# Kernel tuning notes

Hardware: AMD Instinct MI355X
Metric: run time of the kernel (lower is better)

## Reference

```python
import jax, jax.numpy as jnp
import numpy as np

D = 1024
N_HEAD = 16
D_HEAD = D // N_HEAD
EPS = 1e-6


def setup_inputs() -> dict:
    key = jax.random.key(0)
    k1, k2, k3 = jax.random.split(key, 3)
    x = jax.random.normal(k1, (4, 1024, D), dtype=jnp.float32)
    # Linear weights stored as (in, out); y = x @ W
    Wqkv = jax.random.normal(k2, (D, 3 * D), dtype=jnp.float32) * (1.0 / np.sqrt(D))
    Wo = jax.random.normal(k3, (D, D), dtype=jnp.float32) * (1.0 / np.sqrt(D))
    scale_q = jnp.ones((D_HEAD,), dtype=jnp.float32)
    scale_k = jnp.ones((D_HEAD,), dtype=jnp.float32)
    return {"x": x, "Wqkv": Wqkv, "Wo": Wo, "scale_q": scale_q, "scale_k": scale_k}


def _rmsnorm_global(x, scale):
    # NOTE: faithful to source: mean over ALL elements (scalar RMS), not per-vector.
    rms = jnp.sqrt(jnp.mean(x * x))
    return (x / (rms + EPS)) * scale  # scale broadcasts over last dim (d_head)


def reference(x, Wqkv, Wo, scale_q, scale_k):
    b, s, d = x.shape
    qkv = x @ Wqkv  # (b, s, 3d)
    q, k, v = jnp.split(qkv, 3, axis=-1)
    q = q.reshape(b, s, N_HEAD, D_HEAD)
    k = k.reshape(b, s, N_HEAD, D_HEAD)
    v = v.reshape(b, s, N_HEAD, D_HEAD)
    q = _rmsnorm_global(q, scale_q)
    k = _rmsnorm_global(k, scale_k)
    # NOTE: no 1/sqrt(d_head) scaling, no mask (faithful to source)
    attn = jnp.einsum('bqhd,bkhd->bhqk', q, k)
    attn = jax.nn.softmax(attn, axis=-1)
    z = jnp.einsum('bhqk,bkhd->bqhd', attn, v)
    z = z.reshape(b, s, d)
    return z @ Wo
```

## Files before the change

### kernel.cpp

```cpp
#include <hip/hip_runtime.h>

typedef float f32x4 __attribute__((ext_vector_type(4)));
typedef short bf16x8 __attribute__((ext_vector_type(8)));
typedef _Float16 f16x8 __attribute__((ext_vector_type(8)));
typedef unsigned short u16;

__device__ __forceinline__ u16 f2bf(float f) {
  unsigned int u = __float_as_uint(f);
  u = u + 0x7fffu + ((u >> 16) & 1u);
  return (u16)(u >> 16);
}
__device__ __forceinline__ float bf2f(u16 h) {
  return __uint_as_float(((unsigned int)h) << 16);
}
__device__ __forceinline__ u16 f2h(float f) {
  _Float16 h = (_Float16)f;
  union { _Float16 h; u16 u; } cv;
  cv.h = h;
  return cv.u;
}

typedef unsigned int as1_uint __attribute__((address_space(1)));
typedef unsigned int as3_uint __attribute__((address_space(3)));
__device__ __forceinline__ void gl_lds16(const void* g, void* l) {
  __builtin_amdgcn_global_load_lds((as1_uint*)g, (as3_uint*)l, 16, 0, 0);
}


__global__ __launch_bounds__(256) void conv_x_kernel(const float* __restrict__ x,
                                                     u16* __restrict__ Xp) {
  const int g = blockIdx.x * 256 + threadIdx.x;
  const int o = g * 8;
  const int slab = o >> 17;
  const int rem = o & 131071;
  const int kstep = rem >> 12;
  const int rem2 = rem & 4095;
  const int r = rem2 >> 5;
  const int cp = (rem2 & 31) >> 3;
  const int c = cp ^ ((r >> 1) & 3);
  const int s = slab * 128 + r;
  const int k = kstep * 32 + c * 8;
  const float4 v0 = *(const float4*)&x[(size_t)s * 1024 + k];
  const float4 v1 = *(const float4*)&x[(size_t)s * 1024 + k + 4];
  ushort4 a, b;
  a.x = f2h(v0.x); a.y = f2h(v0.y); a.z = f2h(v0.z); a.w = f2h(v0.w);
  b.x = f2h(v1.x); b.y = f2h(v1.y); b.z = f2h(v1.z); b.w = f2h(v1.w);
  *(ushort4*)&Xp[o] = a;
  *(ushort4*)&Xp[o + 4] = b;
}

__global__ __launch_bounds__(256) void conv_w_kernel(
    const float* __restrict__ src, int ncols, u16* __restrict__ dst) {
  __shared__ float tl[64][132];
  const int t = threadIdx.x;
  const int slab = blockIdx.x, kg = blockIdx.y;
  const int n0 = slab * 128, k0 = kg * 64;
#pragma unroll
  for (int i = 0; i < 8; i++) {
    const int fidx = i * 256 + t;
    const int r = fidx >> 5, c4 = (fidx & 31) * 4;
    *(float4*)&tl[r][c4] = *(const float4*)&src[(size_t)(k0 + r) * ncols + n0 + c4];
  }
  __syncthreads();
  const size_t base = (size_t)slab * 131072 + (size_t)(kg * 2) * 4096;
#pragma unroll
  for (int i = 0; i < 4; i++) {
    const int g = i * 256 + t;
    const int img = g >> 9, ci = g & 511;
    const int r = ci >> 2, cp = ci & 3;
    const int c = cp ^ ((r >> 1) & 3);
    const int klc = img * 32 + c * 8;
    ushort4 h0, h1;
    float v[8];
#pragma unroll
    for (int e = 0; e < 8; e++) v[e] = tl[klc + e][r];
    h0.x = f2h(v[0]); h0.y = f2h(v[1]); h0.z = f2h(v[2]); h0.w = f2h(v[3]);
    h1.x = f2h(v[4]); h1.y = f2h(v[5]); h1.z = f2h(v[6]); h1.w = f2h(v[7]);
    *(ushort4*)&dst[base + g * 8] = h0;
    *(ushort4*)&dst[base + g * 8 + 4] = h1;
  }
}

__global__ __launch_bounds__(256) void gemm_qkv_kernel(
    const u16* __restrict__ Xp, const u16* __restrict__ Wp,
    u16* __restrict__ qf, u16* __restrict__ kf, u16* __restrict__ vT,
    const float* __restrict__ scale_q, const float* __restrict__ scale_k,
    float* __restrict__ sums) {
  __shared__ u16 Xs0[4096], Ws0[4096], Xs1[4096], Ws1[4096];
  const int tid = threadIdx.x, wv = tid >> 6, lane = tid & 63;
  const int lm = lane & 15, quad = lane >> 4;
  const int bnS = blockIdx.x, bmS = blockIdx.y;
  const bool is_v = (bnS >= 16);
  const int wr = (wv >> 1) * 64, wc = (wv & 1) * 64;
  const int fq = (quad ^ ((lm >> 1) & 3)) * 8;
  const u16* Xg = Xp + (size_t)bmS * 131072;
  const u16* Wg = Wp + (size_t)bnS * 131072;
  const int dof0 = (wv * 2) * 512, dof1 = (wv * 2 + 1) * 512;
  const f32x4 z4 = {0.f, 0.f, 0.f, 0.f};
  f32x4 acc[4][4];
#pragma unroll
  for (int i = 0; i < 4; i++)
#pragma unroll
    for (int j = 0; j < 4; j++) acc[i][j] = z4;

#define ISSUE(t, Xs, Ws)                                   \
  do {                                                     \
    const size_t tb_ = (size_t)(t) * 4096;                 \
    gl_lds16(Xg + tb_ + dof0 + lane * 8, &Xs[dof0]);       \
    gl_lds16(Xg + tb_ + dof1 + lane * 8, &Xs[dof1]);       \
    gl_lds16(Wg + tb_ + dof0 + lane * 8, &Ws[dof0]);       \
    gl_lds16(Wg + tb_ + dof1 + lane * 8, &Ws[dof1]);       \
  } while (0)

  const u16* A0 = is_v ? Xs0 : Ws0;
  const u16* B0 = is_v ? Ws0 : Xs0;
  const u16* A1 = is_v ? Xs1 : Ws1;
  const u16* B1 = is_v ? Ws1 : Xs1;

  ISSUE(0, Xs0, Ws0);
  for (int t = 0; t < 32; t += 2) {
    __syncthreads();
    {
      f16x8 afr[4], bfr[4];
#pragma unroll
      for (int mi = 0; mi < 4; mi++)
        afr[mi] = *(const f16x8*)&A0[(wr + mi * 16 + lm) * 32 + fq];
#pragma unroll
      for (int ni = 0; ni < 4; ni++)
        bfr[ni] = *(const f16x8*)&B0[(wc + ni * 16 + lm) * 32 + fq];
      ISSUE(t + 1, Xs1, Ws1);
#pragma unroll
      for (int mi = 0; mi < 4; mi++)
#pragma unroll
        for (int ni = 0; ni < 4; ni++)
          acc[mi][ni] = __builtin_amdgcn_mfma_f32_16x16x32_f16(
              afr[mi], bfr[ni], acc[mi][ni], 0, 0, 0);
    }
    __syncthreads();
    {
      f16x8 afr[4], bfr[4];
#pragma unroll
      for (int mi = 0; mi < 4; mi++)
        afr[mi] = *(const f16x8*)&A1[(wr + mi * 16 + lm) * 32 + fq];
#pragma unroll
      for (int ni = 0; ni < 4; ni++)
        bfr[ni] = *(const f16x8*)&B1[(wc + ni * 16 + lm) * 32 + fq];
      if (t + 2 < 32) ISSUE(t + 2, Xs0, Ws0);
#pragma unroll
      for (int mi = 0; mi < 4; mi++)
#pragma unroll
        for (int ni = 0; ni < 4; ni++)
          acc[mi][ni] = __builtin_amdgcn_mfma_f32_16x16x32_f16(
              afr[mi], bfr[ni], acc[mi][ni], 0, 0, 0);
    }
  }
#undef ISSUE

  const int bn = bnS * 128, bm = bmS * 128;
  if (!is_v) {
    const bool is_k = (bnS >= 8);
    u16* dst = is_k ? kf : qf;
    float ss = 0.f;
#pragma unroll
    for (int mi = 0; mi < 4; mi++) {
      const int col0 = bn + wr + mi * 16 + quad * 4;
      const int hh = (col0 >> 6) & 15, d0 = col0 & 63;
      const int dhi = d0 >> 5, cc = (d0 & 31) >> 3, eo = d0 & 7;
      float sc[4] = {1.f, 1.f, 1.f, 1.f};
      if (is_k) {
        const float4 sq = *(const float4*)&scale_q[d0];
        const float4 sk = *(const float4*)&scale_k[d0];
        sc[0] = sq.x * sk.x; sc[1] = sq.y * sk.y;
        sc[2] = sq.z * sk.z; sc[3] = sq.w * sk.w;
      }
#pragma unroll
      for (int ni = 0; ni < 4; ni++) {
        const int s = bm + wc + ni * 16 + lm;
        const int b = s >> 10, sl = s & 1023, st = sl >> 6, r = sl & 63;
        const size_t off = ((size_t)((b * 16 + hh) * 16 + st)) * 4096 +
                           dhi * 2048 + r * 32 + ((cc ^ ((r >> 1) & 3)) * 8) + eo;
        ushort4 h4;
#pragma unroll
        for (int i = 0; i < 4; i++) {
          const float a = acc[mi][ni][i];
          ss += a * a;
          const u16 hv = f2h(a * sc[i]);
          if (i == 0) h4.x = hv;
          else if (i == 1) h4.y = hv;
          else if (i == 2) h4.z = hv;
          else h4.w = hv;
        }
        *(ushort4*)&dst[off] = h4;
      }
    }
#pragma unroll
    for (int m = 32; m >= 1; m >>= 1) ss += __shfl_xor(ss, m, 64);
    if (lane == 0) atomicAdd(&sums[is_k ? 1 : 0], ss);
  } else {
#pragma unroll
    for (int ni = 0; ni < 4; ni++) {
      const int col = (bn - 2048) + wc + ni * 16 + lm;
      const int d = col & 63, hh = col >> 6;
#pragma unroll
      for (int mi = 0; mi < 4; mi++) {
        const int s0 = bm + wr + mi * 16 + quad * 4;
        const int b = s0 >> 10, sl = s0 & 1023, st = sl >> 6;
        const int sh = (sl & 63) >> 5, cc = (sl & 31) >> 3, eo = sl & 7;
        const size_t off = ((size_t)((b * 16 + hh) * 16 + st)) * 4096 +
                           sh * 2048 + d * 32 + ((cc ^ ((d >> 1) & 3)) * 8) + eo;
        ushort4 v4;
        v4.x = f2bf(acc[mi][ni][0]);
        v4.y = f2bf(acc[mi][ni][1]);
        v4.z = f2bf(acc[mi][ni][2]);
        v4.w = f2bf(acc[mi][ni][3]);
        *(ushort4*)&vT[off] = v4;
      }
    }
  }
}

__global__ __launch_bounds__(256) void attn_kernel(
    const u16* __restrict__ qf, const u16* __restrict__ kf,
    const u16* __restrict__ vT, const float* __restrict__ sums,
    u16* __restrict__ z) {
  __shared__ u16 Ks0[4096], Vs0[4096], Ks1[4096], Vs1[4096];
  __shared__ u16 pb[4][2][16][64];
  const int tid = threadIdx.x, wv = tid >> 6, lane = tid & 63;
  const int lm = lane & 15, quad = lane >> 4;
  const int fq = (quad ^ ((lm >> 1) & 3)) * 8;
  const int qt8 = blockIdx.x, hh = blockIdx.y, b = blockIdx.z;
  const float inv_rq = 1.f / (sqrtf(sums[0] * (1.f / 4194304.f)) + 1e-6f);
  const float inv_rk = 1.f / (sqrtf(sums[1] * (1.f / 4194304.f)) + 1e-6f);
  const float cs = inv_rq * inv_rk;
  const size_t hb = ((size_t)(b * 16 + hh)) * 65536;
  const u16* Kg = kf + hb;
  const u16* Vg = vT + hb;
  const int dof = wv * 1024;

  f16x8 aF[2][2];
#pragma unroll
  for (int qs = 0; qs < 2; qs++) {
    const int soff = wv * 32 + qs * 16;
    const size_t qb = hb + (size_t)(qt8 * 2 + (soff >> 6)) * 4096 +
                      (size_t)((soff & 63) + lm) * 32 + fq;
    aF[qs][0] = *(const f16x8*)&qf[qb];
    aF[qs][1] = *(const f16x8*)&qf[qb + 2048];
  }
  const f32x4 zz = {0.f, 0.f, 0.f, 0.f};
  f32x4 zac[2][4];
#pragma unroll
  for (int qs = 0; qs < 2; qs++)
#pragma unroll
    for (int dt = 0; dt < 4; dt++) zac[qs][dt] = zz;
  float rs[2] = {0.f, 0.f};

#define AISSUE(it, Ks, Vs)                                    \
  do {                                                        \
    const size_t tb_ = (size_t)(it) * 4096;                   \
    gl_lds16(Kg + tb_ + dof + lane * 8, &Ks[dof]);            \
    gl_lds16(Kg + tb_ + dof + 512 + lane * 8, &Ks[dof + 512]);\
    gl_lds16(Vg + tb_ + dof + lane * 8, &Vs[dof]);            \
    gl_lds16(Vg + tb_ + dof + 512 + lane * 8, &Vs[dof + 512]);\
  } while (0)

#define ATTN_BODY(it, Ks, Vs, Kn, Vn, do_issue)                               \
  do {                                                                        \
                                         \
    f16x8 kf0[4], kf1[4];                                                     \
    bf16x8 bv[2][4];                                                          \
_Pragma("unroll")                                                             \
    for (int nt = 0; nt < 4; nt++) {                                          \
      const int ro = (nt * 16 + lm) * 32 + fq;                                \
      kf0[nt] = *(const f16x8*)&Ks[ro];                                       \
      kf1[nt] = *(const f16x8*)&Ks[2048 + ro];                                \
    }                                                                         \
_Pragma("unroll")                                                             \
    for (int ch = 0; ch < 2; ch++)                                            \
_Pragma("unroll")                                                             \
      for (int dt = 0; dt < 4; dt++)                                          \
        bv[ch][dt] = *(const bf16x8*)&Vs[ch * 2048 + (dt * 16 + lm) * 32 + fq];\
    if (do_issue) AISSUE((it) + 1, Kn, Vn);                                   \
               \
_Pragma("unroll")                                                             \
    for (int qs = 0; qs < 2; qs++) {                                          \
_Pragma("unroll")                                                             \
      for (int nt = 0; nt < 4; nt++) {                                        \
        f32x4 c = zz;                                                         \
        c = __builtin_amdgcn_mfma_f32_16x16x32_f16(kf0[nt], aF[qs][0], c, 0, 0, 0);\
        c = __builtin_amdgcn_mfma_f32_16x16x32_f16(kf1[nt], aF[qs][1], c, 0, 0, 0);\
        const int k4 = nt * 4 + quad;                                         \
        const int sw = (k4 & 8) | ((k4 ^ lm) & 7);                            \
        ushort4 pw;                                                           \
        float p0 = __expf(c[0] * cs - 60.f);                                  \
        float p1 = __expf(c[1] * cs - 60.f);                                  \
        float p2 = __expf(c[2] * cs - 60.f);                                  \
        float p3 = __expf(c[3] * cs - 60.f);                                  \
        rs[qs] += (p0 + p1) + (p2 + p3);                                      \
        pw.x = f2bf(p0); pw.y = f2bf(p1); pw.z = f2bf(p2); pw.w = f2bf(p3);   \
        *(ushort4*)&pb[wv][qs][lm][sw * 4] = pw;                              \
      }                                                                       \
    }                                                                         \
           \
_Pragma("unroll")                                                             \
    for (int ch = 0; ch < 2; ch++) {                                          \
_Pragma("unroll")                                                             \
      for (int qs = 0; qs < 2; qs++) {                                        \
        const int k4a = ch * 8 + quad * 2, k4b = k4a + 1;                     \
        const ushort4 lo4 =                                                   \
            *(const ushort4*)&pb[wv][qs][lm][((k4a & 8) | ((k4a ^ lm) & 7)) * 4];\
        const ushort4 hi4 =                                                   \
            *(const ushort4*)&pb[wv][qs][lm][((k4b & 8) | ((k4b ^ lm) & 7)) * 4];\
        bf16x8 ap;                                                            \
        ap[0] = (short)lo4.x; ap[1] = (short)lo4.y;                           \
        ap[2] = (short)lo4.z; ap[3] = (short)lo4.w;                           \
        ap[4] = (short)hi4.x; ap[5] = (short)hi4.y;                           \
        ap[6] = (short)hi4.z; ap[7] = (short)hi4.w;                           \
_Pragma("unroll")                                                             \
        for (int dt = 0; dt < 4; dt++)                                        \
          zac[qs][dt] = __builtin_amdgcn_mfma_f32_16x16x32_bf16(              \
              bv[ch][dt], ap, zac[qs][dt], 0, 0, 0);                          \
      }                                                                       \
    }                                                                         \
  } while (0)

  AISSUE(0, Ks0, Vs0);
  for (int it = 0; it < 16; it += 2) {
    __syncthreads();
    ATTN_BODY(it, Ks0, Vs0, Ks1, Vs1, true);
    __syncthreads();
    ATTN_BODY(it + 1, Ks1, Vs1, Ks0, Vs0, (it + 2 < 16));
  }
#undef AISSUE
#undef ATTN_BODY

#pragma unroll
  for (int qs = 0; qs < 2; qs++) {
    rs[qs] += __shfl_xor(rs[qs], 16, 64);
    rs[qs] += __shfl_xor(rs[qs], 32, 64);
  }
  const int slab = b * 8 + qt8;
#pragma unroll
  for (int qs = 0; qs < 2; qs++) {
    const float inv = 1.f / rs[qs];
    const int r = wv * 32 + qs * 16 + lm;
#pragma unroll
    for (int dt = 0; dt < 4; dt++) {
      const int kstep = hh * 2 + (dt >> 1);
      const int d0 = dt * 16 + quad * 4;
      const int cc = (d0 & 31) >> 3, eo = d0 & 7;
      const size_t off = ((size_t)(slab * 32 + kstep)) * 4096 + r * 32 +
                         ((cc ^ ((r >> 1) & 3)) * 8) + eo;
      ushort4 o;
      o.x = f2h(zac[qs][dt][0] * inv);
      o.y = f2h(zac[qs][dt][1] * inv);
      o.z = f2h(zac[qs][dt][2] * inv);
      o.w = f2h(zac[qs][dt][3] * inv);
      *(ushort4*)&z[off] = o;
    }
  }
}

__global__ __launch_bounds__(256) void gemm_o_kernel(const u16* __restrict__ Wop,
                                                     const u16* __restrict__ zp,
                                                     float* __restrict__ out) {
  __shared__ u16 As0[4096], Bs0[4096], As1[4096], Bs1[4096];
  const int tid = threadIdx.x, wv = tid >> 6, lane = tid & 63;
  const int lm = lane & 15, quad = lane >> 4;
  const int wr = (wv >> 1) * 64, wc = (wv & 1) * 64;
  const int fq = (quad ^ ((lm >> 1) & 3)) * 8;
  const u16* Ag = Wop + (size_t)blockIdx.x * 131072;
  const u16* Bg = zp + (size_t)blockIdx.y * 131072;
  const int dof0 = (wv * 2) * 512, dof1 = (wv * 2 + 1) * 512;
  const f32x4 z4 = {0.f, 0.f, 0.f, 0.f};
  f32x4 acc[4][4];
#pragma unroll
  for (int i = 0; i < 4; i++)
#pragma unroll
    for (int j = 0; j < 4; j++) acc[i][j] = z4;

#define ISSUE(t, As, Bs)                                   \
  do {                                                     \
    const size_t tb_ = (size_t)(t) * 4096;                 \
    gl_lds16(Ag + tb_ + dof0 + lane * 8, &As[dof0]);       \
    gl_lds16(Ag + tb_ + dof1 + lane * 8, &As[dof1]);       \
    gl_lds16(Bg + tb_ + dof0 + lane * 8, &Bs[dof0]);       \
    gl_lds16(Bg + tb_ + dof1 + lane * 8, &Bs[dof1]);       \
  } while (0)
#define GBODY(As, Bs)                                                     \
  do {                                                                    \
    f16x8 afr[4], bfr[4];                                                 \
_Pragma("unroll")                                                         \
    for (int mi = 0; mi < 4; mi++)                                        \
      afr[mi] = *(const f16x8*)&As[(wr + mi * 16 + lm) * 32 + fq];        \
_Pragma("unroll")                                                         \
    for (int ni = 0; ni < 4; ni++)                                        \
      bfr[ni] = *(const f16x8*)&Bs[(wc + ni * 16 + lm) * 32 + fq];        \
    DO_ISSUE;                                                             \
_Pragma("unroll")                                                         \
    for (int mi = 0; mi < 4; mi++)                                        \
_Pragma("unroll")                                                         \
      for (int ni = 0; ni < 4; ni++)                                      \
        acc[mi][ni] = __builtin_amdgcn_mfma_f32_16x16x32_f16(             \
            afr[mi], bfr[ni], acc[mi][ni], 0, 0, 0);                      \
  } while (0)

  ISSUE(0, As0, Bs0);
  for (int t = 0; t < 32; t += 2) {
    __syncthreads();
#define DO_ISSUE ISSUE(t + 1, As1, Bs1)
    GBODY(As0, Bs0);
#undef DO_ISSUE
    __syncthreads();
#define DO_ISSUE if (t + 2 < 32) ISSUE(t + 2, As0, Bs0)
    GBODY(As1, Bs1);
#undef DO_ISSUE
  }
#undef ISSUE
#undef GBODY

#pragma unroll
  for (int mi = 0; mi < 4; mi++) {
    const int col0 = blockIdx.x * 128 + wr + mi * 16 + quad * 4;
#pragma unroll
    for (int ni = 0; ni < 4; ni++) {
      const int s = blockIdx.y * 128 + wc + ni * 16 + lm;
      const float4 o = {acc[mi][ni][0], acc[mi][ni][1], acc[mi][ni][2],
                        acc[mi][ni][3]};
      *(float4*)&out[(size_t)s * 1024 + col0] = o;
    }
  }
}

extern "C" void kernel_launch(void* const* d_in, const int* in_sizes, int n_in,
                              void* d_out, int out_size, void* d_ws,
                              size_t ws_size, hipStream_t stream) {
  (void)in_sizes; (void)n_in; (void)out_size; (void)ws_size;
  const float* x = (const float*)d_in[0];
  const float* Wqkv = (const float*)d_in[1];
  const float* Wo = (const float*)d_in[2];
  const float* scale_q = (const float*)d_in[3];
  const float* scale_k = (const float*)d_in[4];
  float* out = (float*)d_out;

  char* ws = (char*)d_ws;
  u16* qf = (u16*)(ws + 0);
  u16* kf = (u16*)(ws + 8388608);
  u16* Xp = (u16*)(ws + 16777216);
  u16* vT = (u16*)(ws + 25165824);
  u16* Wp = (u16*)(ws + 33554432);
  u16* zp = Xp;
  u16* Wop = Wp;
  float* sums = (float*)(ws + 39845888);

  conv_x_kernel<<<2048, 256, 0, stream>>>(x, Xp);
  conv_w_kernel<<<dim3(24, 16), 256, 0, stream>>>(Wqkv, 3072, Wp);
  hipMemsetAsync(sums, 0, 2 * sizeof(float), stream);
  gemm_qkv_kernel<<<dim3(24, 32), 256, 0, stream>>>(Xp, Wp, qf, kf, vT,
                                                    scale_q, scale_k, sums);
  conv_w_kernel<<<dim3(8, 16), 256, 0, stream>>>(Wo, 1024, Wop);
  attn_kernel<<<dim3(8, 16, 4), 256, 0, stream>>>(qf, kf, vT, sums, zp);
  gemm_o_kernel<<<dim3(8, 32), 256, 0, stream>>>(Wop, zp, out);
}
```

Before: 195.4 us.

## Triple-buffer LDS tiles in QKV and output GEMMs with explicit vmcnt waits

Both GEMM kernels switch from a double-buffered LDS ring to a triple-buffered one. Each step now prefetches two tiles ahead and uses an explicit s_waitcnt vmcnt plus a raw s_barrier instead of __syncthreads. The aim is to hide more global-to-LDS latency and cut stalls from the single barrier per step. It raises LDS use per block from 32KB to 48KB, which may lower occupancy, and relies on the vmcnt counts being correct.

```diff
diff --git a/kernel.cpp b/kernel.cpp
--- a/kernel.cpp
+++ b/kernel.cpp
@@ -86,7 +86,7 @@
     u16* __restrict__ qf, u16* __restrict__ kf, u16* __restrict__ vT,
     const float* __restrict__ scale_q, const float* __restrict__ scale_k,
     float* __restrict__ sums) {
-  __shared__ u16 Xs0[4096], Ws0[4096], Xs1[4096], Ws1[4096];
+  __shared__ u16 Xs[3][4096], Ws[3][4096];
   const int tid = threadIdx.x, wv = tid >> 6, lane = tid & 63;
   const int lm = lane & 15, quad = lane >> 4;
   const int bnS = blockIdx.x, bmS = blockIdx.y;
@@ -103,57 +103,48 @@
 #pragma unroll
     for (int j = 0; j < 4; j++) acc[i][j] = z4;
 
-#define ISSUE(t, Xs, Ws)                                   \
+#define ISSUE(t, bi)                                       \
   do {                                                     \
     const size_t tb_ = (size_t)(t) * 4096;                 \
-    gl_lds16(Xg + tb_ + dof0 + lane * 8, &Xs[dof0]);       \
-    gl_lds16(Xg + tb_ + dof1 + lane * 8, &Xs[dof1]);       \
-    gl_lds16(Wg + tb_ + dof0 + lane * 8, &Ws[dof0]);       \
-    gl_lds16(Wg + tb_ + dof1 + lane * 8, &Ws[dof1]);       \
-  } while (0)
-
-  const u16* A0 = is_v ? Xs0 : Ws0;
-  const u16* B0 = is_v ? Ws0 : Xs0;
-  const u16* A1 = is_v ? Xs1 : Ws1;
-  const u16* B1 = is_v ? Ws1 : Xs1;
-
-  ISSUE(0, Xs0, Ws0);
-  for (int t = 0; t < 32; t += 2) {
-    __syncthreads();
-    {
-      f16x8 afr[4], bfr[4];
-#pragma unroll
-      for (int mi = 0; mi < 4; mi++)
-        afr[mi] = *(const f16x8*)&A0[(wr + mi * 16 + lm) * 32 + fq];
-#pragma unroll
-      for (int ni = 0; ni < 4; ni++)
-        bfr[ni] = *(const f16x8*)&B0[(wc + ni * 16 + lm) * 32 + fq];
-      ISSUE(t + 1, Xs1, Ws1);
-#pragma unroll
-      for (int mi = 0; mi < 4; mi++)
-#pragma unroll
-        for (int ni = 0; ni < 4; ni++)
-          acc[mi][ni] = __builtin_amdgcn_mfma_f32_16x16x32_f16(
-              afr[mi], bfr[ni], acc[mi][ni], 0, 0, 0);
-    }
-    __syncthreads();
-    {
-      f16x8 afr[4], bfr[4];
-#pragma unroll
-      for (int mi = 0; mi < 4; mi++)
-        afr[mi] = *(const f16x8*)&A1[(wr + mi * 16 + lm) * 32 + fq];
-#pragma unroll
-      for (int ni = 0; ni < 4; ni++)
-        bfr[ni] = *(const f16x8*)&B1[(wc + ni * 16 + lm) * 32 + fq];
-      if (t + 2 < 32) ISSUE(t + 2, Xs0, Ws0);
-#pragma unroll
-      for (int mi = 0; mi < 4; mi++)
-#pragma unroll
-        for (int ni = 0; ni < 4; ni++)
-          acc[mi][ni] = __builtin_amdgcn_mfma_f32_16x16x32_f16(
-              afr[mi], bfr[ni], acc[mi][ni], 0, 0, 0);
-    }
-  }
+    gl_lds16(Xg + tb_ + dof0 + lane * 8, &Xs[bi][dof0]);   \
+    gl_lds16(Xg + tb_ + dof1 + lane * 8, &Xs[bi][dof1]);   \
+    gl_lds16(Wg + tb_ + dof0 + lane * 8, &Ws[bi][dof0]);   \
+    gl_lds16(Wg + tb_ + dof1 + lane * 8, &Ws[bi][dof1]);   \
+  } while (0)
+
+#define BODY(t, bi, WN, DOISS)                                              \
+  do {                                                                      \
+    asm volatile("s_waitcnt vmcnt(" #WN ")" ::: "memory");                  \
+    __builtin_amdgcn_s_barrier();                                           \
+    asm volatile("" ::: "memory");                                          \
+    if (DOISS) ISSUE((t) + 2, ((bi) + 2) % 3);                              \
+    const u16* A_ = is_v ? &Xs[bi][0] : &Ws[bi][0];                         \
+    const u16* B_ = is_v ? &Ws[bi][0] : &Xs[bi][0];                         \
+    f16x8 afr[4], bfr[4];                                                   \
+    _Pragma("unroll")                                                       \
+    for (int mi = 0; mi < 4; mi++)                                          \
+      afr[mi] = *(const f16x8*)&A_[(wr + mi * 16 + lm) * 32 + fq];          \
+    _Pragma("unroll")                                                       \
+    for (int ni = 0; ni < 4; ni++)                                          \
+      bfr[ni] = *(const f16x8*)&B_[(wc + ni * 16 + lm) * 32 + fq];          \
+    _Pragma("unroll")                                                       \
+    for (int mi = 0; mi < 4; mi++)                                          \
+      _Pragma("unroll")                                                     \
+      for (int ni = 0; ni < 4; ni++)                                        \
+        acc[mi][ni] = __builtin_amdgcn_mfma_f32_16x16x32_f16(               \
+            afr[mi], bfr[ni], acc[mi][ni], 0, 0, 0);                        \
+  } while (0)
+
+  ISSUE(0, 0);
+  ISSUE(1, 1);
+  for (int t = 0; t < 30; t += 3) {
+    BODY(t, 0, 4, true);
+    BODY(t + 1, 1, 4, true);
+    BODY(t + 2, 2, 4, true);
+  }
+  BODY(30, 0, 4, false);
+  BODY(31, 1, 0, false);
+#undef BODY
 #undef ISSUE
 
   const int bn = bnS * 128, bm = bmS * 128;
@@ -363,7 +354,7 @@
 __global__ __launch_bounds__(256) void gemm_o_kernel(const u16* __restrict__ Wop,
                                                      const u16* __restrict__ zp,
                                                      float* __restrict__ out) {
-  __shared__ u16 As0[4096], Bs0[4096], As1[4096], Bs1[4096];
+  __shared__ u16 As[3][4096], Bs[3][4096];
   const int tid = threadIdx.x, wv = tid >> 6, lane = tid & 63;
   const int lm = lane & 15, quad = lane >> 4;
   const int wr = (wv >> 1) * 64, wc = (wv & 1) * 64;
@@ -378,45 +369,47 @@
 #pragma unroll
     for (int j = 0; j < 4; j++) acc[i][j] = z4;
 
-#define ISSUE(t, As, Bs)                                   \
+#define ISSUE(t, bi)                                       \
   do {                                                     \
     const size_t tb_ = (size_t)(t) * 4096;                 \
-    gl_lds16(Ag + tb_ + dof0 + lane * 8, &As[dof0]);       \
-    gl_lds16(Ag + tb_ + dof1 + lane * 8, &As[dof1]);       \
-    gl_lds16(Bg + tb_ + dof0 + lane * 8, &Bs[dof0]);       \
-    gl_lds16(Bg + tb_ + dof1 + lane * 8, &Bs[dof1]);       \
-  } while (0)
-#define GBODY(As, Bs)                                                     \
-  do {                                                                    \
-    f16x8 afr[4], bfr[4];                                                 \
-_Pragma("unroll")                                                         \
-    for (int mi = 0; mi < 4; mi++)                                        \
-      afr[mi] = *(const f16x8*)&As[(wr + mi * 16 + lm) * 32 + fq];        \
-_Pragma("unroll")                                                         \
-    for (int ni = 0; ni < 4; ni++)                                        \
-      bfr[ni] = *(const f16x8*)&Bs[(wc + ni * 16 + lm) * 32 + fq];        \
-    DO_ISSUE;                                                             \
-_Pragma("unroll")                                                         \
-    for (int mi = 0; mi < 4; mi++)                                        \
-_Pragma("unroll")                                                         \
-      for (int ni = 0; ni < 4; ni++)                                      \
-        acc[mi][ni] = __builtin_amdgcn_mfma_f32_16x16x32_f16(             \
-            afr[mi], bfr[ni], acc[mi][ni], 0, 0, 0);                      \
-  } while (0)
-
-  ISSUE(0, As0, Bs0);
-  for (int t = 0; t < 32; t += 2) {
-    __syncthreads();
-#define DO_ISSUE ISSUE(t + 1, As1, Bs1)
-    GBODY(As0, Bs0);
-#undef DO_ISSUE
-    __syncthreads();
-#define DO_ISSUE if (t + 2 < 32) ISSUE(t + 2, As0, Bs0)
-    GBODY(As1, Bs1);
-#undef DO_ISSUE
-  }
+    gl_lds16(Ag + tb_ + dof0 + lane * 8, &As[bi][dof0]);   \
+    gl_lds16(Ag + tb_ + dof1 + lane * 8, &As[bi][dof1]);   \
+    gl_lds16(Bg + tb_ + dof0 + lane * 8, &Bs[bi][dof0]);   \
+    gl_lds16(Bg + tb_ + dof1 + lane * 8, &Bs[bi][dof1]);   \
+  } while (0)
+
+#define BODY(t, bi, WN, DOISS)                                              \
+  do {                                                                      \
+    asm volatile("s_waitcnt vmcnt(" #WN ")" ::: "memory");                  \
+    __builtin_amdgcn_s_barrier();                                           \
+    asm volatile("" ::: "memory");                                          \
+    if (DOISS) ISSUE((t) + 2, ((bi) + 2) % 3);                              \
+    f16x8 afr[4], bfr[4];                                                   \
+    _Pragma("unroll")                                                       \
+    for (int mi = 0; mi < 4; mi++)                                          \
+      afr[mi] = *(const f16x8*)&As[bi][(wr + mi * 16 + lm) * 32 + fq];      \
+    _Pragma("unroll")                                                       \
+    for (int ni = 0; ni < 4; ni++)                                          \
+      bfr[ni] = *(const f16x8*)&Bs[bi][(wc + ni * 16 + lm) * 32 + fq];      \
+    _Pragma("unroll")                                                       \
+    for (int mi = 0; mi < 4; mi++)                                          \
+      _Pragma("unroll")                                                     \
+      for (int ni = 0; ni < 4; ni++)                                        \
+        acc[mi][ni] = __builtin_amdgcn_mfma_f32_16x16x32_f16(               \
+            afr[mi], bfr[ni], acc[mi][ni], 0, 0, 0);                        \
+  } while (0)
+
+  ISSUE(0, 0);
+  ISSUE(1, 1);
+  for (int t = 0; t < 30; t += 3) {
+    BODY(t, 0, 4, true);
+    BODY(t + 1, 1, 4, true);
+    BODY(t + 2, 2, 4, true);
+  }
+  BODY(30, 0, 4, false);
+  BODY(31, 1, 0, false);
+#undef BODY
 #undef ISSUE
-#undef GBODY
 
 #pragma unroll
   for (int mi = 0; mi < 4; mi++) {
```

After: 204.0 us. 4.4% more time.
